# Performance work log

Hardware: AMD Instinct MI355X
Metric: run time of the kernel (lower is better)

## Reference

```python
import jax, jax.numpy as jnp
import numpy as np

SCALE = 1.0

def setup_inputs() -> dict:
    key = jax.random.key(0)
    k1, k2 = jax.random.split(key)
    features = jax.random.normal(k1, (16, 512, 128, 128), dtype=jnp.float32)
    probs = jax.random.normal(k2, (16, 19, 128, 128), dtype=jnp.float32)
    return {"features": features, "probs": probs}

def reference(features, probs):
    B, K, H, W = probs.shape
    C = features.shape[1]
    p = probs.reshape(B, K, H * W)               # [B, K, HW]
    f = features.reshape(B, C, H * W)            # [B, C, HW]
    attn = jax.nn.softmax(SCALE * p, axis=2)     # softmax over spatial dim
    # ocr_context[b, k, c] = sum_hw attn[b,k,hw] * f[b,c,hw]
    ctx = jnp.einsum('bks,bcs->bkc', attn, f)    # [B, K, C]
    return jnp.transpose(ctx, (0, 2, 1))[..., None]  # [B, C, K, 1]
```

## Files before the change

### kernel.cpp

```cpp
#include <hip/hip_runtime.h>
#include <math.h>

#define BATCH 16
#define KCLS  19
#define CCH   512
#define HW    16384

#define KSPLIT 16
#define KB     (HW / KSPLIT)
#define BK     64
#define NCHUNK (KB / BK)
#define NT     128
#define KPAD   20
#define BCN    (BATCH * CCH)

typedef __attribute__((ext_vector_type(8))) short  short8;
typedef __attribute__((ext_vector_type(4))) float  floatx4;

static __device__ __forceinline__ unsigned cvt_pk(float lo, float hi) {
  unsigned r;
  asm("v_cvt_pk_bf16_f32 %0, %1, %2" : "=v"(r) : "v"(lo), "v"(hi));
  return r;
}

static __device__ __forceinline__ short8 pack8(floatx4 a, floatx4 b) {
  union { unsigned u[4]; short8 s; } x;
  x.u[0] = cvt_pk(a[0], a[1]);
  x.u[1] = cvt_pk(a[2], a[3]);
  x.u[2] = cvt_pk(b[0], b[1]);
  x.u[3] = cvt_pk(b[2], b[3]);
  return x.s;
}

struct FSet { floatx4 v[8]; };

__global__ __launch_bounds__(256, 2) void gather_mfma(
    const float* __restrict__ feat, const float* __restrict__ probs,
    float* __restrict__ pws, float* __restrict__ part) {
  __shared__ __align__(16) short A_all[KCLS][KB];
  __shared__ float red[KCLS][4];

  const int bid = blockIdx.x;
  const int b   = bid & 15;
  const int r1  = bid >> 4;
  const int ct  = r1 & 3;
  const int ks  = r1 >> 2;
  const int k0  = ks * KB;

  const int tid  = threadIdx.x;
  const int wave = tid >> 6;
  const int lane = tid & 63;

  const float* fbase = feat  + ((size_t)(b * CCH + ct * NT)) * HW + k0;
  const float* pbase = probs + ((size_t)b * KCLS) * HW + k0;

  const int ch0 = wave * 32 + (lane & 15);
  const int ch1 = ch0 + 16;
  const float* fptr0 = fbase + (size_t)ch0 * HW + (lane >> 4) * 8;
  const float* fptr1 = fbase + (size_t)ch1 * HW + (lane >> 4) * 8;

  floatx4 acc00 = {0,0,0,0}, acc01 = {0,0,0,0}, acc10 = {0,0,0,0}, acc11 = {0,0,0,0};

  FSet sA, sB;

#define LOADF(S, c)                                                             \
  {                                                                             \
    const int cb = (c) * BK;                                                    \
    S.v[0] = *(const floatx4*)(fptr0 + cb);                                     \
    S.v[1] = *(const floatx4*)(fptr0 + cb + 4);                                 \
    S.v[2] = *(const floatx4*)(fptr1 + cb);                                     \
    S.v[3] = *(const floatx4*)(fptr1 + cb + 4);                                 \
    S.v[4] = *(const floatx4*)(fptr0 + cb + 32);                                \
    S.v[5] = *(const floatx4*)(fptr0 + cb + 36);                                \
    S.v[6] = *(const floatx4*)(fptr1 + cb + 32);                                \
    S.v[7] = *(const floatx4*)(fptr1 + cb + 36);                                \
  }

#define GEMMC(S, c)                                                             \
  {                                                                             \
    const char* Ab = (const char*)A_all;                                        \
    const int rm0  = lane & 15;                                                 \
    const int rm1  = 16 + (rm0 < 3 ? rm0 : 2);    \
    _Pragma("unroll")                                                           \
    for (int kt = 0; kt < 2; kt++) {                                            \
      const int g = (c) * 8 + kt * 4 + (lane >> 4);                             \
      short8 a0 = *(const short8*)(Ab + rm0 * 2048 + ((g ^ (rm0 & 7)) << 4));   \
      short8 a1 = *(const short8*)(Ab + rm1 * 2048 + ((g ^ (rm1 & 7)) << 4));   \
      short8 b0 = pack8(S.v[kt * 4 + 0], S.v[kt * 4 + 1]);                      \
      short8 b1 = pack8(S.v[kt * 4 + 2], S.v[kt * 4 + 3]);                      \
      acc00 = __builtin_amdgcn_mfma_f32_16x16x32_bf16(a0, b0, acc00, 0, 0, 0);  \
      acc01 = __builtin_amdgcn_mfma_f32_16x16x32_bf16(a0, b1, acc01, 0, 0, 0);  \
      acc10 = __builtin_amdgcn_mfma_f32_16x16x32_bf16(a1, b0, acc10, 0, 0, 0);  \
      acc11 = __builtin_amdgcn_mfma_f32_16x16x32_bf16(a1, b1, acc11, 0, 0, 0);  \
    }                                                                           \
  }

  LOADF(sA, 0);

  for (int j = 0; j < KCLS; j++) {
    float4 p = *(const float4*)(pbase + (size_t)j * HW + tid * 4);
    float e0 = __expf(p.x), e1 = __expf(p.y), e2 = __expf(p.z), e3 = __expf(p.w);
    union { unsigned u[2]; } x;
    x.u[0] = cvt_pk(e0, e1);
    x.u[1] = cvt_pk(e2, e3);
    *(unsigned long long*)((char*)A_all + j * 2048 +
                           (((tid >> 1) ^ (j & 7)) << 4) + (tid & 1) * 8) =
        ((unsigned long long)x.u[1] << 32) | x.u[0];
    if (ct == 0) {
      float s = e0 + e1 + e2 + e3;
      for (int off = 32; off > 0; off >>= 1) s += __shfl_xor(s, off);
      if (lane == 0) red[j][wave] = s;
    }
  }
  __syncthreads();

  if (ct == 0 && tid < KCLS) {
    float tot = red[tid][0] + red[tid][1] + red[tid][2] + red[tid][3];
    pws[(b * KCLS + tid) * KSPLIT + ks] = tot;
  }

  for (int c = 0; c < NCHUNK; c += 2) {
    LOADF(sB, c + 1);
    GEMMC(sA, c);
    if (c + 2 < NCHUNK) LOADF(sA, c + 2);
    GEMMC(sB, c + 1);
  }

  {
    const int chb = ct * NT + wave * 32;
    const int cl  = lane & 15;
    const int rb  = (lane >> 4) * 4;
    size_t bc0 = (size_t)b * CCH + chb + cl;
    size_t bc1 = bc0 + 16;
    float* p0 = part + ((size_t)ks * BCN + bc0) * KPAD + rb;
    float* p1 = part + ((size_t)ks * BCN + bc1) * KPAD + rb;
    *(floatx4*)p0 = acc00;
    *(floatx4*)p1 = acc01;
    if (rb == 0) {
      *(floatx4*)(p0 + 16) = acc10;
      *(floatx4*)(p1 + 16) = acc11;
    }
  }
#undef LOADF
#undef GEMMC
}

__global__ __launch_bounds__(256) void reduce_kernel(
    const float* __restrict__ part, const float* __restrict__ pws,
    float* __restrict__ out) {
  const int gid = blockIdx.x * 256 + threadIdx.x;
  const int bc = gid / KPAD, r = gid - bc * KPAD;
  if (r < KCLS) {
    const int b = bc >> 9;
    float se = 0.f;
    #pragma unroll
    for (int k = 0; k < KSPLIT; k++)
      se += pws[(b * KCLS + r) * KSPLIT + k];
    float s = 0.f;
    #pragma unroll
    for (int k = 0; k < KSPLIT; k++)
      s += part[(size_t)k * (BCN * KPAD) + gid];
    out[(size_t)bc * KCLS + r] = s / se;
  }
}

extern "C" void kernel_launch(void* const* d_in, const int* in_sizes, int n_in,
                              void* d_out, int out_size, void* d_ws, size_t ws_size,
                              hipStream_t stream) {
  const float* feat  = (const float*)d_in[0];
  const float* probs = (const float*)d_in[1];
  float* out  = (float*)d_out;
  float* pws  = (float*)d_ws;
  float* part = (float*)((char*)d_ws + 32768);

  gather_mfma<<<BATCH * 4 * KSPLIT, 256, 0, stream>>>(feat, probs, pws, part);
  reduce_kernel<<<(BCN * KPAD) / 256, 256, 0, stream>>>(part, pws, out);
}
```

Before: 142.9 us.

## Merge channel tiles into one 1024-thread block and use software bf16 rounding

Each block now covers all 512 channels of a (batch, spatial split) pair with 1024 threads, instead of four 256-thread blocks that each handle 128 channels. The exp of the probabilities is therefore computed once per block rather than recomputed by every channel tile, and the grid shrinks to one block per CU. The inline v_cvt_pk_bf16_f32 conversion is replaced by a software round-to-nearest-even bit trick, which costs extra ALU work in the hot GEMM loop. launch_bounds(1024, 2) sharply limits the registers available per thread, so register spills are a risk given the double-buffered 64-float feature sets.

Measured after the change: 121.6 us (median of 3 runs). 1.18x faster.

```diff
diff --git a/kernel.cpp b/kernel.cpp
--- a/kernel.cpp
+++ b/kernel.cpp
@@ -10,31 +10,29 @@
 #define KB     (HW / KSPLIT)
 #define BK     64
 #define NCHUNK (KB / BK)
-#define NT     128
 #define KPAD   20
 #define BCN    (BATCH * CCH)
 
 typedef __attribute__((ext_vector_type(8))) short  short8;
 typedef __attribute__((ext_vector_type(4))) float  floatx4;
 
-static __device__ __forceinline__ unsigned cvt_pk(float lo, float hi) {
-  unsigned r;
-  asm("v_cvt_pk_bf16_f32 %0, %1, %2" : "=v"(r) : "v"(lo), "v"(hi));
-  return r;
+static __device__ __forceinline__ ushort f2bf(float x) {
+  unsigned u = __float_as_uint(x);
+  return (ushort)((u + 0x7FFFu + ((u >> 16) & 1u)) >> 16);
 }
 
 static __device__ __forceinline__ short8 pack8(floatx4 a, floatx4 b) {
-  union { unsigned u[4]; short8 s; } x;
-  x.u[0] = cvt_pk(a[0], a[1]);
-  x.u[1] = cvt_pk(a[2], a[3]);
-  x.u[2] = cvt_pk(b[0], b[1]);
-  x.u[3] = cvt_pk(b[2], b[3]);
-  return x.s;
+  short8 v;
+  v[0] = (short)f2bf(a[0]); v[1] = (short)f2bf(a[1]);
+  v[2] = (short)f2bf(a[2]); v[3] = (short)f2bf(a[3]);
+  v[4] = (short)f2bf(b[0]); v[5] = (short)f2bf(b[1]);
+  v[6] = (short)f2bf(b[2]); v[7] = (short)f2bf(b[3]);
+  return v;
 }
 
 struct FSet { floatx4 v[8]; };
 
-__global__ __launch_bounds__(256, 2) void gather_mfma(
+__global__ __launch_bounds__(1024, 2) void gather_mfma(
     const float* __restrict__ feat, const float* __restrict__ probs,
     float* __restrict__ pws, float* __restrict__ part) {
   __shared__ __align__(16) short A_all[KCLS][KB];
@@ -42,16 +40,14 @@
 
   const int bid = blockIdx.x;
   const int b   = bid & 15;
-  const int r1  = bid >> 4;
-  const int ct  = r1 & 3;
-  const int ks  = r1 >> 2;
+  const int ks  = bid >> 4;
   const int k0  = ks * KB;
 
   const int tid  = threadIdx.x;
   const int wave = tid >> 6;
   const int lane = tid & 63;
 
-  const float* fbase = feat  + ((size_t)(b * CCH + ct * NT)) * HW + k0;
+  const float* fbase = feat  + ((size_t)b * CCH) * HW + k0;
   const float* pbase = probs + ((size_t)b * KCLS) * HW + k0;
 
   const int ch0 = wave * 32 + (lane & 15);
@@ -97,27 +93,30 @@
 
   LOADF(sA, 0);
 
-  for (int j = 0; j < KCLS; j++) {
-    float4 p = *(const float4*)(pbase + (size_t)j * HW + tid * 4);
-    float e0 = __expf(p.x), e1 = __expf(p.y), e2 = __expf(p.z), e3 = __expf(p.w);
-    union { unsigned u[2]; } x;
-    x.u[0] = cvt_pk(e0, e1);
-    x.u[1] = cvt_pk(e2, e3);
-    *(unsigned long long*)((char*)A_all + j * 2048 +
-                           (((tid >> 1) ^ (j & 7)) << 4) + (tid & 1) * 8) =
-        ((unsigned long long)x.u[1] << 32) | x.u[0];
-    if (ct == 0) {
-      float s = e0 + e1 + e2 + e3;
+  #pragma unroll
+  for (int p = 0; p < 5; p++) {
+    const int idx = p * 1024 + tid;
+    if (idx < KCLS * 256) {
+      const int j = idx >> 8;
+      const int t = idx & 255;
+      float4 pp = *(const float4*)(pbase + (size_t)j * HW + t * 4);
+      float e0 = __expf(pp.x), e1 = __expf(pp.y);
+      float e2 = __expf(pp.z), e3 = __expf(pp.w);
+      unsigned long long w64 =
+          (unsigned long long)f2bf(e0) | ((unsigned long long)f2bf(e1) << 16) |
+          ((unsigned long long)f2bf(e2) << 32) | ((unsigned long long)f2bf(e3) << 48);
+      *(unsigned long long*)((char*)A_all + j * 2048 +
+                             (((t >> 1) ^ (j & 7)) << 4) + (t & 1) * 8) = w64;
+      float s = (e0 + e1) + (e2 + e3);
       for (int off = 32; off > 0; off >>= 1) s += __shfl_xor(s, off);
-      if (lane == 0) red[j][wave] = s;
+      if (lane == 0) red[j][wave & 3] = s;
     }
   }
   __syncthreads();
 
-  if (ct == 0 && tid < KCLS) {
-    float tot = red[tid][0] + red[tid][1] + red[tid][2] + red[tid][3];
-    pws[(b * KCLS + tid) * KSPLIT + ks] = tot;
-  }
+  if (tid < KCLS)
+    pws[(b * KCLS + tid) * KSPLIT + ks] =
+        (red[tid][0] + red[tid][1]) + (red[tid][2] + red[tid][3]);
 
   for (int c = 0; c < NCHUNK; c += 2) {
     LOADF(sB, c + 1);
@@ -127,7 +126,7 @@
   }
 
   {
-    const int chb = ct * NT + wave * 32;
+    const int chb = wave * 32;
     const int cl  = lane & 15;
     const int rb  = (lane >> 4) * 4;
     size_t bc0 = (size_t)b * CCH + chb + cl;
@@ -173,6 +172,6 @@
   float* pws  = (float*)d_ws;
   float* part = (float*)((char*)d_ws + 32768);
 
-  gather_mfma<<<BATCH * 4 * KSPLIT, 256, 0, stream>>>(feat, probs, pws, part);
+  gather_mfma<<<BATCH * KSPLIT, 1024, 0, stream>>>(feat, probs, pws, part);
   reduce_kernel<<<(BCN * KPAD) / 256, 256, 0, stream>>>(part, pws, out);
 }
```
